# Performance work log

Hardware: AMD Instinct MI355X
Metric: run time of the kernel (lower is better)

## Reference

```python
import jax, jax.numpy as jnp
import numpy as np

EPS = 1e-5
GROUPS = 8


def setup_inputs() -> dict:
    key = jax.random.key(0)
    ks = jax.random.split(key, 7)
    B, C, H, W = 4, 512, 64, 64
    x = jax.random.normal(ks[0], (B, C, H, W), dtype=jnp.float32)
    gn_w = jax.random.normal(ks[1], (C,), dtype=jnp.float32) * 0.02 + 1.0
    gn_b = jax.random.normal(ks[2], (C,), dtype=jnp.float32) * 0.02
    # 1x1 convs stored as [out, in] matrices
    qkv_w = jax.random.normal(ks[3], (3 * C, C), dtype=jnp.float32) * (C ** -0.5)
    qkv_b = jax.random.normal(ks[4], (3 * C,), dtype=jnp.float32) * 0.02
    proj_w = jax.random.normal(ks[5], (C, C), dtype=jnp.float32) * (C ** -0.5)
    proj_b = jax.random.normal(ks[6], (C,), dtype=jnp.float32) * 0.02
    return {"x": x, "gn_w": gn_w, "gn_b": gn_b, "qkv_w": qkv_w,
            "qkv_b": qkv_b, "proj_w": proj_w, "proj_b": proj_b}


def _group_norm(x, w, b):
    B, C, H, W = x.shape
    xg = x.reshape(B, GROUPS, C // GROUPS, H, W)
    mu = jnp.mean(xg, axis=(2, 3, 4), keepdims=True)
    var = jnp.var(xg, axis=(2, 3, 4), keepdims=True)
    xn = ((xg - mu) * jax.lax.rsqrt(var + EPS)).reshape(B, C, H, W)
    return xn * w[None, :, None, None] + b[None, :, None, None]


def reference(x, gn_w, gn_b, qkv_w, qkv_b, proj_w, proj_b):
    B, C, H, W = x.shape
    N = H * W
    scale = C ** (-0.5)
    h = _group_norm(x, gn_w, gn_b)
    # 1x1 conv -> [B, 3C, N]
    qkv = jnp.einsum('oc,bcn->bon', qkv_w, h.reshape(B, C, N)) + qkv_b[None, :, None]
    q, k, v = jnp.split(qkv, 3, axis=1)  # each [B, C, N]
    # scores[b, n, m] = sum_c q[b,c,n] * k[b,c,m]
    attn = jax.nn.softmax(jnp.einsum('bcn,bcm->bnm', q, k) * scale, axis=-1)
    # out[b,c,n] = sum_m v[b,c,m] * attn[b,n,m]   (v @ attn^T)
    hout = jnp.einsum('bcm,bnm->bcn', v, attn)
    proj = jnp.einsum('oc,bcn->bon', proj_w, hout) + proj_b[None, :, None]
    return x + proj.reshape(B, C, H, W)
```

## Files before the change

### kernel.cpp

```cpp
#include <hip/hip_runtime.h>
#include <math.h>

#define SCALE 0.044194173824159216f
#define QI 28.22222222f
#define K8SCL ((4.5f/127.0f)*(4.5f/127.0f)*SCALE)
#define K8SCL2 (K8SCL * 1.4426950408889634f)
#define PSCL 0.49609375f
#define VSCL 0.035433070866141736f

typedef __bf16 bf16x8 __attribute__((ext_vector_type(8)));
typedef float  f32x4  __attribute__((ext_vector_type(4)));
typedef int    i32x4  __attribute__((ext_vector_type(4)));
typedef unsigned int u32;

__device__ __forceinline__ void gload16(const void* g, void* l) {
    __builtin_amdgcn_global_load_lds(
        (const __attribute__((address_space(1))) u32*)g,
        (__attribute__((address_space(3))) u32*)l, 16, 0, 0);
}

__global__ __launch_bounds__(256) void gn_part_w(const float* __restrict__ x,
                                                 float* __restrict__ part,
                                                 const float* __restrict__ qw,
                                                 const float* __restrict__ pwsrc,
                                                 __bf16* __restrict__ wdst) {
    if (blockIdx.x >= 512) {
        int i = ((blockIdx.x - 512)*256 + threadIdx.x) * 4;
        #pragma unroll
        for (int rep = 0; rep < 4; ++rep, i += 262144) {
            const float* src = (i < 786432) ? (qw + i) : (pwsrc + (i - 786432));
            float4 v = *(const float4*)src;
            wdst[i+0] = (__bf16)v.x; wdst[i+1] = (__bf16)v.y;
            wdst[i+2] = (__bf16)v.z; wdst[i+3] = (__bf16)v.w;
        }
        return;
    }
    int gi = blockIdx.x >> 4, sl = blockIdx.x & 15;
    const float4* p = (const float4*)(x + (size_t)gi * 64 * 4096) + (size_t)sl * 4096;
    float s = 0.f, ss = 0.f;
    #pragma unroll 4
    for (int i = threadIdx.x; i < 4096; i += 256) {
        float4 v = p[i];
        s  += v.x + v.y + v.z + v.w;
        ss += v.x*v.x + v.y*v.y + v.z*v.z + v.w*v.w;
    }
    __shared__ float rs[256], rss[256];
    rs[threadIdx.x] = s; rss[threadIdx.x] = ss;
    __syncthreads();
    for (int o = 128; o > 0; o >>= 1) {
        if (threadIdx.x < o) { rs[threadIdx.x] += rs[threadIdx.x+o]; rss[threadIdx.x] += rss[threadIdx.x+o]; }
        __syncthreads();
    }
    if (threadIdx.x == 0) {
        part[blockIdx.x*2 + 0] = rs[0];
        part[blockIdx.x*2 + 1] = rss[0];
    }
}

__global__ __launch_bounds__(64) void gn_fin(const float* __restrict__ part,
                                             float* __restrict__ stats) {
    int t = threadIdx.x;
    if (t < 32) {
        float s = 0.f, ss = 0.f;
        #pragma unroll
        for (int i = 0; i < 16; ++i) { s += part[(t*16+i)*2]; ss += part[(t*16+i)*2+1]; }
        float inv = 1.0f / (float)(64 * 4096);
        float mu  = s * inv;
        float var = ss * inv - mu * mu;
        stats[t*2 + 0] = mu;
        stats[t*2 + 1] = rsqrtf(var + 1e-5f);
    }
}

__global__ __launch_bounds__(256) void gn_apply_t(const float* __restrict__ x,
                                                  const float* __restrict__ stats,
                                                  const float* __restrict__ gw,
                                                  const float* __restrict__ gb,
                                                  __bf16* __restrict__ hT) {
    __shared__ __bf16 tile[64][88];
    int b = blockIdx.z, c0 = blockIdx.y * 64, n0 = blockIdx.x * 64;
    int t = threadIdx.x;
    float mu  = stats[(b*8 + blockIdx.y)*2];
    float rsg = stats[(b*8 + blockIdx.y)*2 + 1];
    int c = t >> 2, ns = t & 3;
    float a = gw[c0+c] * rsg;
    float d = gb[c0+c] - mu * a;
    const float* xr = x + ((size_t)b*512 + c0 + c)*4096 + n0 + ns*16;
    #pragma unroll
    for (int e4 = 0; e4 < 4; ++e4) {
        float4 v = *(const float4*)(xr + e4*4);
        tile[ns*16 + e4*4 + 0][c] = (__bf16)(v.x*a + d);
        tile[ns*16 + e4*4 + 1][c] = (__bf16)(v.y*a + d);
        tile[ns*16 + e4*4 + 2][c] = (__bf16)(v.z*a + d);
        tile[ns*16 + e4*4 + 3][c] = (__bf16)(v.w*a + d);
    }
    __syncthreads();
    int n = t >> 2, cs = t & 3;
    __bf16* dst = hT + ((size_t)b*4096 + n0 + n)*512 + c0 + cs*16;
    *(uint4*)(dst)     = *(const uint4*)(&tile[n][cs*16]);
    *(uint4*)(dst + 8) = *(const uint4*)(&tile[n][cs*16 + 8]);
}

template<int MODE>
__global__ __launch_bounds__(256) void mm128(
        const __bf16* __restrict__ A, int lda, size_t sA,
        const __bf16* __restrict__ B, int ldb, size_t sB,
        int Kdim,
        const float* __restrict__ bias,
        const float* __restrict__ res, size_t sR,
        void* __restrict__ out, int ldo, size_t sO) {
    __shared__ __bf16 As[3][128][32];
    __shared__ __bf16 Bs[3][128][32];

    const int t = threadIdx.x, w = t >> 6, l = t & 63;
    const int l15 = l & 15, lq = l >> 4;
    const int bz = blockIdx.z;

    const int gx = gridDim.x;
    int lin = blockIdx.y * gx + blockIdx.x;
    {
        const int nwg = gx * gridDim.y;
        const int qn = nwg >> 3, rn = nwg & 7;
        const int xcd = lin & 7, idx = lin >> 3;
        const int base = (xcd < rn) ? xcd*(qn+1) : rn*(qn+1) + (xcd-rn)*qn;
        lin = base + idx;
    }
    const int j0 = (lin % gx) * 128;
    const int i0 = (lin / gx) * 128;

    const __bf16* Ab = A + sA*bz;
    const __bf16* Bb = B + sB*bz;
    const int rowblk = (w & 1)*64;
    const int colblk = (w >> 1)*64;

    const int slot0 = w*64 + l;
    const int rowS0 = slot0 >> 2;
    const int rowS1 = rowS0 + 64;
    const int csS   = (((slot0 & 3) ^ ((rowS0 >> 1) & 3))) * 8;
    const int off0  = (w*64)*16;
    const int off1  = (256 + w*64)*16;

    f32x4 acc[4][4];
    #pragma unroll
    for (int mr = 0; mr < 4; ++mr)
        #pragma unroll
        for (int nr = 0; nr < 4; ++nr)
            #pragma unroll
            for (int r = 0; r < 4; ++r) acc[mr][nr][r] = 0.f;

    auto STAGE = [&](int kc, int bi) {
        char* Ad = (char*)As[bi];
        char* Bd = (char*)Bs[bi];
        gload16(Ab + (size_t)(i0 + rowS0)*lda + kc + csS, Ad + off0);
        gload16(Ab + (size_t)(i0 + rowS1)*lda + kc + csS, Ad + off1);
        gload16(Bb + (size_t)(j0 + rowS0)*ldb + kc + csS, Bd + off0);
        gload16(Bb + (size_t)(j0 + rowS1)*ldb + kc + csS, Bd + off1);
    };

    const int rsw = (l15 >> 1) & 3;
    const int koff = (lq ^ rsw) << 4;

    const int nch = Kdim >> 5;
    STAGE(0, 0);
    STAGE(32, 1);

    for (int cc = 0; cc < nch; ++cc) {
        if (cc < nch - 1) asm volatile("s_waitcnt vmcnt(4)\n\ts_barrier" ::: "memory");
        else              asm volatile("s_waitcnt vmcnt(0)\n\ts_barrier" ::: "memory");

        const char* Ac = (const char*)As[cc % 3];
        const char* Bc = (const char*)Bs[cc % 3];
        bf16x8 av[4], bv[4];
        #pragma unroll
        for (int mr = 0; mr < 4; ++mr)
            av[mr] = *(const bf16x8*)(Ac + (rowblk + mr*16 + l15)*64 + koff);
        #pragma unroll
        for (int nr = 0; nr < 4; ++nr)
            bv[nr] = *(const bf16x8*)(Bc + (colblk + nr*16 + l15)*64 + koff);
        if (cc + 2 < nch) STAGE((cc + 2)*32, (cc + 2) % 3);
        #pragma unroll
        for (int mr = 0; mr < 4; ++mr)
            #pragma unroll
            for (int nr = 0; nr < 4; ++nr)
                acc[mr][nr] = __builtin_amdgcn_mfma_f32_16x16x32_bf16(av[mr], bv[nr], acc[mr][nr], 0, 0, 0);
    }

    #pragma unroll
    for (int mr = 0; mr < 4; ++mr)
        #pragma unroll
        for (int nr = 0; nr < 4; ++nr) {
            int col = j0 + colblk + nr*16 + l15;
            #pragma unroll
            for (int r = 0; r < 4; ++r) {
                int lrow = rowblk + mr*16 + lq*4 + r;
                int gi = i0 + lrow;
                float v = acc[mr][nr][r];
                if constexpr (MODE == 1) {
                    v += bias[gi];
                    int q = __float2int_rn(v * QI);
                    q = q < -127 ? -127 : (q > 127 ? 127 : q);
                    ((char*)out)[sO*bz + (size_t)gi*ldo + col] = (char)q;
                } else {
                    v += bias[gi] + res[sR*bz + (size_t)gi*ldo + col];
                    ((float*)out)[sO*bz + (size_t)gi*ldo + col] = v;
                }
            }
        }
}

template<int M> struct AccT { using T = f32x4; };
template<> struct AccT<4> { using T = i32x4; };
template<> struct AccT<5> { using T = i32x4; };

#define LDSB (98304 + 4096)
template<int MODE>
__global__ __launch_bounds__(512) void mm256(
        const void* __restrict__ A, int ldaB, size_t sAB,
        const void* __restrict__ B, int ldbB, size_t sBB,
        int Kbytes,
        const float* __restrict__ bias,
        void* __restrict__ out, int ldo, size_t sO,
        float* __restrict__ rowpart) {
    extern __shared__ char smem[];
    char*  Abase = smem;
    char*  Bbase = smem + 49152;
    float* redp  = (float*)(smem + 98304);
    char*  ptile = smem;

    const int t = threadIdx.x, w = t >> 6, l = t & 63;
    const int l15 = l & 15, lq = l >> 4;
    const int bz = (MODE == 4) ? (blockIdx.z >> 1) : blockIdx.z;
    const int kh = (MODE == 4) ? (blockIdx.z & 1) : 0;
    const size_t kbase = (size_t)kh * Kbytes;

    const int gx = gridDim.x;
    int lin = blockIdx.y * gx + blockIdx.x;
    {
        const int nwg = gx * gridDim.y;
        const int qn = nwg >> 3, rn = nwg & 7;
        const int xcd = lin & 7, idx = lin >> 3;
        const int base = (xcd < rn) ? xcd*(qn+1) : rn*(qn+1) + (xcd-rn)*qn;
        lin = base + idx;
    }
    const int j0 = (lin % gx) * 256;
    const int i0 = (lin / gx) * 256;

    const char* Ab = (const char*)A + sAB*bz + kbase;
    const char* Bb = (const char*)B + sBB*bz + kbase;
    const int wr = w & 1;
    const int wc = w >> 1;

    const int slot0 = w*64 + l;
    const int rowS0 = slot0 >> 2;
    const int rowS1 = rowS0 + 128;
    const int csS   = (((slot0 & 3) ^ ((rowS0 >> 1) & 3))) * 16;
    const int off0  = (w*64)*16;
    const int off1  = (512 + w*64)*16;

    typename AccT<MODE>::T acc[8][4];
    #pragma unroll
    for (int mr = 0; mr < 8; ++mr)
        #pragma unroll
        for (int nr = 0; nr < 4; ++nr)
            #pragma unroll
            for (int r = 0; r < 4; ++r) acc[mr][nr][r] = 0;

    auto STAGE = [&](int kc, int bi) {
        char* Ad = Abase + bi*16384;
        char* Bd = Bbase + bi*16384;
        gload16(Ab + (size_t)(i0 + rowS0)*ldaB + kc + csS, Ad + off0);
        gload16(Ab + (size_t)(i0 + rowS1)*ldaB + kc + csS, Ad + off1);
        gload16(Bb + (size_t)(j0 + rowS0)*ldbB + kc + csS, Bd + off0);
        gload16(Bb + (size_t)(j0 + rowS1)*ldbB + kc + csS, Bd + off1);
    };

    const int rsw = (l15 >> 1) & 3;
    const int koff = (lq ^ rsw) << 4;

    const int nch = Kbytes >> 6;
    STAGE(0, 0);
    STAGE(64, 1);

    for (int cc = 0; cc < nch; ++cc) {
        if (cc < nch - 1) asm volatile("s_waitcnt vmcnt(4)\n\ts_barrier" ::: "memory");
        else              asm volatile("s_waitcnt vmcnt(0)\n\ts_barrier" ::: "memory");

        const char* Ac = Abase + (cc % 3)*16384;
        const char* Bc = Bbase + (cc % 3)*16384;
        i32x4 araw[8], braw[4];
        #pragma unroll
        for (int mr = 0; mr < 8; ++mr)
            araw[mr] = *(const i32x4*)(Ac + (wr*128 + mr*16 + l15)*64 + koff);
        #pragma unroll
        for (int nr = 0; nr < 4; ++nr)
            braw[nr] = *(const i32x4*)(Bc + (wc*64 + nr*16 + l15)*64 + koff);
        if (cc + 2 < nch) STAGE((cc + 2)*64, (cc + 2) % 3);
        #pragma unroll
        for (int mr = 0; mr < 8; ++mr)
            #pragma unroll
            for (int nr = 0; nr < 4; ++nr) {
                if constexpr (MODE == 4 || MODE == 5) {
                    acc[mr][nr] = __builtin_amdgcn_mfma_i32_16x16x64_i8(
                        araw[mr], braw[nr], acc[mr][nr], 0, 0, 0);
                } else {
                    acc[mr][nr] = __builtin_amdgcn_mfma_f32_16x16x32_bf16(
                        __builtin_bit_cast(bf16x8, araw[mr]),
                        __builtin_bit_cast(bf16x8, braw[nr]), acc[mr][nr], 0, 0, 0);
                }
            }
    }

    if constexpr (MODE == 5) {
        const int jblk = j0 >> 8;
        float rpart[8][4];
        #pragma unroll
        for (int mr = 0; mr < 8; ++mr)
            #pragma unroll
            for (int r = 0; r < 4; ++r) rpart[mr][r] = 0.f;
        __syncthreads();
        #pragma unroll
        for (int mr = 0; mr < 8; ++mr)
            #pragma unroll
            for (int nr = 0; nr < 4; ++nr) {
                int colL = wc*64 + nr*16 + l15;
                #pragma unroll
                for (int r = 0; r < 4; ++r) {
                    int row = wr*128 + mr*16 + lq*4 + r;
                    float e = exp2f((float)acc[mr][nr][r] * K8SCL2);
                    int q = __float2int_rn(e * PSCL);
                    if (q > 127) q = 127;
                    ptile[row*272 + colL] = (char)q;
                    rpart[mr][r] += (float)q;
                }
            }
        #pragma unroll
        for (int m = 1; m < 16; m <<= 1)
            #pragma unroll
            for (int mr = 0; mr < 8; ++mr)
                #pragma unroll
                for (int r = 0; r < 4; ++r)
                    rpart[mr][r] += __shfl_xor(rpart[mr][r], m);
        if (l15 == 0) {
            #pragma unroll
            for (int mr = 0; mr < 8; ++mr)
                #pragma unroll
                for (int r = 0; r < 4; ++r)
                    redp[(wr*128 + mr*16 + lq*4 + r)*4 + wc] = rpart[mr][r];
        }
        __syncthreads();
        {
            int row = t >> 1, half = t & 1;
            const char* src = ptile + row*272 + half*128;
            char* dst = (char*)out + sO*bz + (size_t)(i0 + row)*ldo + j0 + half*128;
            #pragma unroll
            for (int i = 0; i < 8; ++i)
                *(uint4*)(dst + i*16) = *(const uint4*)(src + i*16);
        }
        if (t < 256)
            rowpart[(size_t)bz*131072 + (size_t)jblk*4096 + i0 + t] =
                redp[t*4+0] + redp[t*4+1] + redp[t*4+2] + redp[t*4+3];
        return;
    }

    if constexpr (MODE == 0) {
        __syncthreads();
        #pragma unroll
        for (int mr = 0; mr < 8; ++mr)
            #pragma unroll
            for (int nr = 0; nr < 4; ++nr) {
                int colL = wc*64 + nr*16 + l15;
                float b = bias[j0 + colL];
                #pragma unroll
                for (int r = 0; r < 4; ++r) {
                    int row = wr*128 + mr*16 + lq*4 + r;
                    float v = (float)acc[mr][nr][r] + b;
                    int q = __float2int_rn(v * QI);
                    q = q < -127 ? -127 : (q > 127 ? 127 : q);
                    ptile[row*272 + colL] = (char)q;
                }
            }
        __syncthreads();
        int row = t >> 1, half = t & 1;
        int colg = j0 + half*128;
        const char* src = ptile + row*272 + half*128;
        char* qk = (char*)out + (size_t)bz*8388608;
        char* dst = (colg < 512) ? (qk + (size_t)(i0 + row)*512 + colg)
                                 : (qk + 2097152 + (size_t)(i0 + row)*512 + (colg - 512));
        #pragma unroll
        for (int i = 0; i < 8; ++i)
            *(uint4*)(dst + i*16) = *(const uint4*)(src + i*16);
        return;
    }

    #pragma unroll
    for (int mr = 0; mr < 8; ++mr)
        #pragma unroll
        for (int nr = 0; nr < 4; ++nr) {
            int col = j0 + wc*64 + nr*16 + l15;
            #pragma unroll
            for (int r = 0; r < 4; ++r) {
                int lrow = wr*128 + mr*16 + lq*4 + r;
                __bf16* po = (__bf16*)out + sO*bz + (size_t)kh*2097152;
                po[(size_t)(i0 + lrow)*ldo + col] = (__bf16)(float)acc[mr][nr][r];
            }
        }
}

__global__ __launch_bounds__(256) void pv_reduce(const __bf16* __restrict__ part,
                                                 const float* __restrict__ rowpart,
                                                 __bf16* __restrict__ OT) {
    int b = blockIdx.y, r0 = blockIdx.x * 16;
    __shared__ float rs[16];
    int t = threadIdx.x;
    if (t < 16) {
        const float* rp = rowpart + (size_t)b*131072 + r0 + t;
        float s = 0.f;
        #pragma unroll
        for (int jb = 0; jb < 16; ++jb) s += rp[jb*4096];
        rs[t] = VSCL / s;
    }
    __syncthreads();
    int row = r0 + (t >> 4), cseg = (t & 15) * 32;
    const __bf16* p0 = part + (size_t)b*16777216 + (size_t)row*512 + cseg;
    const __bf16* p1 = p0 + 2097152;
    __bf16* o = OT + (size_t)b*2097152 + (size_t)row*512 + cseg;
    float sc = rs[t >> 4];
    #pragma unroll
    for (int g = 0; g < 4; ++g) {
        bf16x8 a = *(const bf16x8*)(p0 + g*8);
        bf16x8 bb = *(const bf16x8*)(p1 + g*8);
        bf16x8 r;
        #pragma unroll
        for (int e = 0; e < 8; ++e) r[e] = (__bf16)(((float)a[e] + (float)bb[e]) * sc);
        *(bf16x8*)(o + g*8) = r;
    }
}

extern "C" void kernel_launch(void* const* d_in, const int* in_sizes, int n_in,
                              void* d_out, int out_size, void* d_ws, size_t ws_size,
                              hipStream_t stream) {
    const float* x      = (const float*)d_in[0];
    const float* gn_w   = (const float*)d_in[1];
    const float* gn_b   = (const float*)d_in[2];
    const float* qkv_w  = (const float*)d_in[3];
    const float* qkv_b  = (const float*)d_in[4];
    const float* proj_w = (const float*)d_in[5];
    const float* proj_b = (const float*)d_in[6];

    char* w8 = (char*)d_ws;
    char*   v8buf = w8 + 33554432;
    __bf16* OT   = (__bf16*)(w8 + 50331648);
    __bf16* wq   = (__bf16*)(w8 + 67108864);
    __bf16* pw   = (__bf16*)(w8 + 68681728);
    float*  rowpart = (float*)(w8 + 69206016);
    float*  part = (float*)(w8 + 71303168);
    float*  st   = (float*)(w8 + 71307264);
    const size_t baseP = 71307520ULL;
    __bf16* hT   = (__bf16*)(w8 + baseP);

    size_t avail = (ws_size > baseP) ? (ws_size - baseP) : 0;
    int cap = (int)(avail / 33554432ULL);
    if (cap < 1) cap = 1;
    if (cap > 4) cap = 4;

    hipFuncSetAttribute((const void*)mm256<0>,
                        hipFuncAttributeMaxDynamicSharedMemorySize, LDSB);
    hipFuncSetAttribute((const void*)mm256<4>,
                        hipFuncAttributeMaxDynamicSharedMemorySize, LDSB);
    hipFuncSetAttribute((const void*)mm256<5>,
                        hipFuncAttributeMaxDynamicSharedMemorySize, LDSB);

    gn_part_w<<<768, 256, 0, stream>>>(x, part, qkv_w, proj_w, wq);
    gn_fin<<<1, 64, 0, stream>>>(part, st);
    gn_apply_t<<<dim3(64, 8, 4), 256, 0, stream>>>(x, st, gn_w, gn_b, hT);

    mm256<0><<<dim3(4, 16, 4), 512, LDSB, stream>>>(
        hT, 1024, (size_t)4096*1024, wq, 1024, 0, 1024,
        qkv_b, w8, 0, 0, nullptr);
    mm128<1><<<dim3(32, 4, 4), 256, 0, stream>>>(
        wq + (size_t)1024*512, 512, 0, hT, 512, (size_t)4096*512, 512,
        qkv_b + 1024, nullptr, 0, v8buf, 4096, (size_t)512*4096);

    for (int b0 = 0; b0 < 4; b0 += cap) {
        int c = (4 - b0 < cap) ? (4 - b0) : cap;
        char* Pb = w8 + baseP + (size_t)b0*33554432;
        mm256<5><<<dim3(16, 16, c), 512, LDSB, stream>>>(
            w8 + (size_t)b0*8388608, 512, 8388608,
            w8 + (size_t)b0*8388608 + 2097152, 512, 8388608, 512,
            nullptr, Pb, 4096, 33554432,
            rowpart + (size_t)b0*131072);
        mm256<4><<<dim3(2, 16, c*2), 512, LDSB, stream>>>(
            Pb, 4096, 33554432,
            v8buf + (size_t)b0*2097152, 4096, 2097152, 2048,
            nullptr, Pb + 16777216, 512, 16777216,
            nullptr);
        pv_reduce<<<dim3(256, c), 256, 0, stream>>>(
            (const __bf16*)(Pb + 16777216), rowpart + (size_t)b0*131072,
            OT + (size_t)b0*2097152);
    }

    mm128<2><<<dim3(32, 4, 4), 256, 0, stream>>>(
        pw, 512, 0, OT, 512, (size_t)4096*512, 512,
        proj_b, x, (size_t)512*4096, (float*)d_out, 4096, (size_t)512*4096);
}
```

Baseline: 219.1 us.

## Split PV matmul K four ways and drop LDS-staged epilogue stores

The P·V int8 matmul now splits K into four slices instead of two. That doubles the number of workgroups, and pv_reduce is extended to sum four bf16 partials. The epilogues of the QK/softmax and QKV kernels no longer stage the quantized tile in shared memory for 16-byte vector stores. They write bytes directly to global memory from the accumulator layout. This removes a barrier and an LDS round trip, but it risks poorly coalesced byte-wide global stores and adds extra partial-sum traffic.

```diff
diff --git a/kernel.cpp b/kernel.cpp
--- a/kernel.cpp
+++ b/kernel.cpp
@@ -225,12 +225,11 @@
     char*  Abase = smem;
     char*  Bbase = smem + 49152;
     float* redp  = (float*)(smem + 98304);
-    char*  ptile = smem;
 
     const int t = threadIdx.x, w = t >> 6, l = t & 63;
     const int l15 = l & 15, lq = l >> 4;
-    const int bz = (MODE == 4) ? (blockIdx.z >> 1) : blockIdx.z;
-    const int kh = (MODE == 4) ? (blockIdx.z & 1) : 0;
+    const int bz = (MODE == 4) ? (blockIdx.z >> 2) : blockIdx.z;
+    const int kh = (MODE == 4) ? (blockIdx.z & 3) : 0;
     const size_t kbase = (size_t)kh * Kbytes;
 
     const int gx = gridDim.x;
@@ -317,19 +316,18 @@
         for (int mr = 0; mr < 8; ++mr)
             #pragma unroll
             for (int r = 0; r < 4; ++r) rpart[mr][r] = 0.f;
-        __syncthreads();
         #pragma unroll
         for (int mr = 0; mr < 8; ++mr)
             #pragma unroll
             for (int nr = 0; nr < 4; ++nr) {
-                int colL = wc*64 + nr*16 + l15;
+                int col = j0 + wc*64 + nr*16 + l15;
                 #pragma unroll
                 for (int r = 0; r < 4; ++r) {
                     int row = wr*128 + mr*16 + lq*4 + r;
                     float e = exp2f((float)acc[mr][nr][r] * K8SCL2);
                     int q = __float2int_rn(e * PSCL);
                     if (q > 127) q = 127;
-                    ptile[row*272 + colL] = (char)q;
+                    ((char*)out)[sO*bz + (size_t)(i0 + row)*ldo + col] = (char)q;
                     rpart[mr][r] += (float)q;
                 }
             }
@@ -340,6 +338,7 @@
                 #pragma unroll
                 for (int r = 0; r < 4; ++r)
                     rpart[mr][r] += __shfl_xor(rpart[mr][r], m);
+        __syncthreads();
         if (l15 == 0) {
             #pragma unroll
             for (int mr = 0; mr < 8; ++mr)
@@ -348,60 +347,33 @@
                     redp[(wr*128 + mr*16 + lq*4 + r)*4 + wc] = rpart[mr][r];
         }
         __syncthreads();
-        {
-            int row = t >> 1, half = t & 1;
-            const char* src = ptile + row*272 + half*128;
-            char* dst = (char*)out + sO*bz + (size_t)(i0 + row)*ldo + j0 + half*128;
-            #pragma unroll
-            for (int i = 0; i < 8; ++i)
-                *(uint4*)(dst + i*16) = *(const uint4*)(src + i*16);
-        }
         if (t < 256)
             rowpart[(size_t)bz*131072 + (size_t)jblk*4096 + i0 + t] =
                 redp[t*4+0] + redp[t*4+1] + redp[t*4+2] + redp[t*4+3];
         return;
     }
 
-    if constexpr (MODE == 0) {
-        __syncthreads();
-        #pragma unroll
-        for (int mr = 0; mr < 8; ++mr)
-            #pragma unroll
-            for (int nr = 0; nr < 4; ++nr) {
-                int colL = wc*64 + nr*16 + l15;
-                float b = bias[j0 + colL];
-                #pragma unroll
-                for (int r = 0; r < 4; ++r) {
-                    int row = wr*128 + mr*16 + lq*4 + r;
-                    float v = (float)acc[mr][nr][r] + b;
+    #pragma unroll
+    for (int mr = 0; mr < 8; ++mr)
+        #pragma unroll
+        for (int nr = 0; nr < 4; ++nr) {
+            int col = j0 + wc*64 + nr*16 + l15;
+            #pragma unroll
+            for (int r = 0; r < 4; ++r) {
+                int lrow = wr*128 + mr*16 + lq*4 + r;
+                if constexpr (MODE == 0) {
+                    float v = (float)acc[mr][nr][r] + bias[col];
                     int q = __float2int_rn(v * QI);
                     q = q < -127 ? -127 : (q > 127 ? 127 : q);
-                    ptile[row*272 + colL] = (char)q;
+                    char* qk = (char*)out + (size_t)bz*8388608;
+                    size_t row = (size_t)(i0 + lrow);
+                    char* p = (col < 512) ? (qk + row*512 + col)
+                                          : (qk + 2097152 + row*512 + (col - 512));
+                    *p = (char)q;
+                } else {
+                    __bf16* po = (__bf16*)out + sO*bz + (size_t)kh*2097152;
+                    po[(size_t)(i0 + lrow)*ldo + col] = (__bf16)(float)acc[mr][nr][r];
                 }
-            }
-        __syncthreads();
-        int row = t >> 1, half = t & 1;
-        int colg = j0 + half*128;
-        const char* src = ptile + row*272 + half*128;
-        char* qk = (char*)out + (size_t)bz*8388608;
-        char* dst = (colg < 512) ? (qk + (size_t)(i0 + row)*512 + colg)
-                                 : (qk + 2097152 + (size_t)(i0 + row)*512 + (colg - 512));
-        #pragma unroll
-        for (int i = 0; i < 8; ++i)
-            *(uint4*)(dst + i*16) = *(const uint4*)(src + i*16);
-        return;
-    }
-
-    #pragma unroll
-    for (int mr = 0; mr < 8; ++mr)
-        #pragma unroll
-        for (int nr = 0; nr < 4; ++nr) {
-            int col = j0 + wc*64 + nr*16 + l15;
-            #pragma unroll
-            for (int r = 0; r < 4; ++r) {
-                int lrow = wr*128 + mr*16 + lq*4 + r;
-                __bf16* po = (__bf16*)out + sO*bz + (size_t)kh*2097152;
-                po[(size_t)(i0 + lrow)*ldo + col] = (__bf16)(float)acc[mr][nr][r];
             }
         }
 }
@@ -422,16 +394,18 @@
     __syncthreads();
     int row = r0 + (t >> 4), cseg = (t & 15) * 32;
     const __bf16* p0 = part + (size_t)b*16777216 + (size_t)row*512 + cseg;
-    const __bf16* p1 = p0 + 2097152;
     __bf16* o = OT + (size_t)b*2097152 + (size_t)row*512 + cseg;
     float sc = rs[t >> 4];
     #pragma unroll
     for (int g = 0; g < 4; ++g) {
-        bf16x8 a = *(const bf16x8*)(p0 + g*8);
-        bf16x8 bb = *(const bf16x8*)(p1 + g*8);
+        bf16x8 a0 = *(const bf16x8*)(p0 + g*8);
+        bf16x8 a1 = *(const bf16x8*)(p0 + 2097152 + g*8);
+        bf16x8 a2 = *(const bf16x8*)(p0 + 4194304 + g*8);
+        bf16x8 a3 = *(const bf16x8*)(p0 + 6291456 + g*8);
         bf16x8 r;
         #pragma unroll
-        for (int e = 0; e < 8; ++e) r[e] = (__bf16)(((float)a[e] + (float)bb[e]) * sc);
+        for (int e = 0; e < 8; ++e)
+            r[e] = (__bf16)((((float)a0[e] + (float)a1[e]) + ((float)a2[e] + (float)a3[e])) * sc);
         *(bf16x8*)(o + g*8) = r;
     }
 }
@@ -489,9 +463,9 @@
             w8 + (size_t)b0*8388608 + 2097152, 512, 8388608, 512,
             nullptr, Pb, 4096, 33554432,
             rowpart + (size_t)b0*131072);
-        mm256<4><<<dim3(2, 16, c*2), 512, LDSB, stream>>>(
+        mm256<4><<<dim3(2, 16, c*4), 512, LDSB, stream>>>(
             Pb, 4096, 33554432,
-            v8buf + (size_t)b0*2097152, 4096, 2097152, 2048,
+            v8buf + (size_t)b0*2097152, 4096, 2097152, 1024,
             nullptr, Pb + 16777216, 512, 16777216,
             nullptr);
         pv_reduce<<<dim3(256, c), 256, 0, stream>>>(
```

After: 209.1 us. -4.5%, faster.
